# Kernel optimization log

Measured on AMD Instinct MI355X. Metric: run time of the kernel, lower is better.

Reference implementation:

```python
import jax, jax.numpy as jnp
import numpy as np

# pseudo_image_dims = [512, 512] -> canvas_x = dims[0], canvas_y = dims[1]
CANVAS_X = 512
CANVAS_Y = 512
SHIFT_SIZE = 2          # gen_index_shift(2, ...) -> 5x5 neighborhood
VR_THRESH = 0.1
B = 2
N_LI = 1_000_000
N_RA = 500_000


def setup_inputs() -> dict:
    key = jax.random.key(0)
    k1, k2, k3, k4 = jax.random.split(key, 4)
    li_input = jax.random.normal(k1, (B, N_LI, 4), dtype=jnp.float32)
    ra_input = jax.random.normal(k2, (B, N_RA, 5), dtype=jnp.float32)
    # voxel_coords (y, x) per valid point; batch column is implicitly 0
    li_coords = jax.random.randint(k3, (B, N_LI, 2), 0, CANVAS_Y).astype(jnp.int32)
    ra_coords = jax.random.randint(k4, (B, N_RA, 2), 0, CANVAS_Y).astype(jnp.int32)
    # all points valid; identity point_idxes (deterministic scatter)
    li_point_idxes = jnp.broadcast_to(jnp.arange(N_LI, dtype=jnp.int32), (B, N_LI))
    ra_point_idxes = jnp.broadcast_to(jnp.arange(N_RA, dtype=jnp.int32), (B, N_RA))
    return {
        "li_input": li_input,
        "li_coords": li_coords,
        "li_point_idxes": li_point_idxes,
        "ra_input": ra_input,
        "ra_coords": ra_coords,
        "ra_point_idxes": ra_point_idxes,
    }


def _per_batch(li_pts, li_coor, li_valid, ra_pts, ra_coor, ra_valid):
    X, Y = CANVAS_X, CANVAS_Y
    # flat BEV index per valid point: y * canvas_x + x, scattered to full point set
    li_flat = (li_coor[:, 0] * X + li_coor[:, 1]).astype(jnp.int32)
    li_ind = jnp.zeros(li_pts.shape[0], jnp.int32).at[li_valid].set(li_flat)
    ra_flat = (ra_coor[:, 0] * X + ra_coor[:, 1]).astype(jnp.int32)
    ra_ind = jnp.zeros(ra_pts.shape[0], jnp.int32).at[ra_valid].set(ra_flat)

    vr = jnp.abs(ra_pts[:, 4])
    ra_dy = vr > VR_THRESH

    # DynamicScatter(average_points=False): per-voxel MAX of |vr|; a voxel is
    # dynamic if its max |vr| > 0.1. Empty voxels -> -inf identity -> not dynamic.
    vox_max = jax.ops.segment_max(vr[ra_valid], ra_flat, num_segments=Y * X)
    dyn = (vox_max > VR_THRESH).reshape(Y, X)

    # expand each dynamic voxel to its 5x5 neighborhood with the original's
    # wrap logic: y is modded by (dims[0]+1), x by (dims[1]+1); shifted cells
    # landing on the extra row/col (== dim) are dropped.
    ys = jnp.arange(Y, dtype=jnp.int32)[:, None]   # [Y,1]
    xs = jnp.arange(X, dtype=jnp.int32)[None, :]   # [1,X]
    neigh = jnp.zeros(Y * X, dtype=jnp.int32)
    for i in range(-SHIFT_SIZE, SHIFT_SIZE + 1):
        for j in range(-SHIFT_SIZE, SHIFT_SIZE + 1):
            sy = (ys + i) % (X + 1)   # grid_size[0] = pseudo_image_dims[0] + 1
            sx = (xs + j) % (Y + 1)   # grid_size[1] = pseudo_image_dims[1] + 1
            valid = dyn & (sy < Y) & (sx < X)      # [Y,X]
            flat = sy * X + sx                      # [Y,X]
            flat = jnp.where(valid, flat, 0)
            neigh = neigh.at[flat.reshape(-1)].max(valid.reshape(-1).astype(jnp.int32))
    neigh_mask = neigh > 0          # [Y*X] bool

    li_dy = neigh_mask[li_ind]      # points with matching flat index become dynamic
    return li_dy, li_ind, ra_dy, ra_ind


def reference(li_input, li_coords, li_point_idxes, ra_input, ra_coords, ra_point_idxes):
    return jax.vmap(_per_batch)(li_input, li_coords, li_point_idxes,
                                ra_input, ra_coords, ra_point_idxes)
```

## Files before the change

kernel.cpp:

```cpp
#include <hip/hip_runtime.h>
#include <hip/hip_bf16.h>

#define CANVAS 512
#define PLANE (CANVAS * CANVAS)
#define GRIDW 513
#define BATCH 2
#define N_LI 1000000
#define N_RA 500000

__global__ void zero_dyn(uint32_t* __restrict__ p, int nwords) {
    int i = blockIdx.x * blockDim.x + threadIdx.x;
    if (i < nwords) p[i] = 0u;
}

__global__ void ra_kernel(const float* __restrict__ ra_input,
                          const int*   __restrict__ ra_coords,
                          int* __restrict__ ra_dy_out,
                          int* __restrict__ ra_ind_out,
                          unsigned char* __restrict__ dyn) {
    int idx = blockIdx.x * blockDim.x + threadIdx.x;
    if (idx >= BATCH * N_RA) return;
    float vr = fabsf(ra_input[(size_t)idx * 5 + 4]);
    int2 c = ((const int2*)ra_coords)[idx];
    int flat = c.x * CANVAS + c.y;
    int dy = (vr > 0.1f) ? 1 : 0;
    ra_dy_out[idx]  = dy;
    ra_ind_out[idx] = flat;
    if (dy) {
        int b = idx / N_RA;
        dyn[(size_t)b * PLANE + flat] = 1;
    }
}

__global__ void dilate_kernel(const unsigned char* __restrict__ dyn,
                              unsigned char* __restrict__ neigh) {
    int idx = blockIdx.x * blockDim.x + threadIdx.x;
    if (idx >= BATCH * PLANE) return;
    int b    = idx / PLANE;
    int cell = idx - b * PLANE;
    int ty = cell >> 9;
    int tx = cell & (CANVAS - 1);
    const unsigned char* d = dyn + (size_t)b * PLANE;

    int sys[5]; int nsy = 0;
    int sxs[5]; int nsx = 0;
#pragma unroll
    for (int off = -2; off <= 2; ++off) {
        int sy = ty - off;
        if (sy < 0) sy += GRIDW;
        if (sy >= GRIDW) sy -= GRIDW;
        if (sy < CANVAS) { sys[nsy++] = sy; }
        int sx = tx - off;
        if (sx < 0) sx += GRIDW;
        if (sx >= GRIDW) sx -= GRIDW;
        if (sx < CANVAS) { sxs[nsx++] = sx; }
    }
    int acc = 0;
    for (int a = 0; a < nsy; ++a) {
        int base = sys[a] * CANVAS;
        for (int c2 = 0; c2 < nsx; ++c2) acc |= d[base + sxs[c2]];
    }
    neigh[idx] = (unsigned char)(acc ? 1 : 0);
}

__global__ void li_kernel(const int* __restrict__ li_coords,
                          const unsigned char* __restrict__ neigh,
                          int* __restrict__ li_dy_out,
                          int* __restrict__ li_ind_out) {
    int idx = blockIdx.x * blockDim.x + threadIdx.x;
    if (idx >= BATCH * N_LI) return;
    int2 c = ((const int2*)li_coords)[idx];
    int flat = c.x * CANVAS + c.y;
    int b = idx / N_LI;
    li_ind_out[idx] = flat;
    li_dy_out[idx]  = neigh[(size_t)b * PLANE + flat] ? 1 : 0;
}

extern "C" void kernel_launch(void* const* d_in, const int* in_sizes, int n_in,
                              void* d_out, int out_size, void* d_ws, size_t ws_size,
                              hipStream_t stream) {
    const int*   li_coords = (const int*)d_in[1];
    const float* ra_input  = (const float*)d_in[3];
    const int*   ra_coords = (const int*)d_in[4];

    int* out        = (int*)d_out;
    int* li_dy_out  = out;
    int* li_ind_out = out + (size_t)BATCH * N_LI;
    int* ra_dy_out  = out + (size_t)2 * BATCH * N_LI;
    int* ra_ind_out = out + (size_t)2 * BATCH * N_LI + (size_t)BATCH * N_RA;

    unsigned char* dyn   = (unsigned char*)d_ws;
    unsigned char* neigh = dyn + (size_t)BATCH * PLANE;

    const int nwords = BATCH * PLANE / 4;
    zero_dyn<<<(nwords + 255) / 256, 256, 0, stream>>>((uint32_t*)dyn, nwords);
    ra_kernel<<<(BATCH * N_RA + 255) / 256, 256, 0, stream>>>(
        ra_input, ra_coords, ra_dy_out, ra_ind_out, dyn);
    dilate_kernel<<<(BATCH * PLANE + 255) / 256, 256, 0, stream>>>(dyn, neigh);
    li_kernel<<<(BATCH * N_LI + 255) / 256, 256, 0, stream>>>(
        li_coords, neigh, li_dy_out, li_ind_out);
}
```

Baseline: 141.8 us.

## Bit-pack neighbor mask, process two points per thread with vector nontemporal IO

The dilated neighbor mask is packed into 32-bit words with a wavefront ballot, so the lidar lookup gathers from a 64KB-per-batch bitmap instead of a byte plane. The radar and lidar kernels each handle two points per thread, using 16-byte coordinate loads and 8-byte nontemporal stores. The dilate loop is branchless and fully unrolled. The aim is to cut memory traffic and cache pressure on the random gathers, in exchange for extra bit arithmetic and an assumption that the wavefront is 64 lanes wide.

```diff
diff --git a/kernel.cpp b/kernel.cpp
--- a/kernel.cpp
+++ b/kernel.cpp
@@ -1,79 +1,102 @@
 #include <hip/hip_runtime.h>
-#include <hip/hip_bf16.h>
 
 #define CANVAS 512
 #define PLANE (CANVAS * CANVAS)
+#define WORDS (PLANE / 32)
 #define GRIDW 513
 #define BATCH 2
 #define N_LI 1000000
 #define N_RA 500000
+
+typedef int int2v __attribute__((ext_vector_type(2)));
+typedef int int4v __attribute__((ext_vector_type(4)));
 
 __global__ void zero_dyn(uint32_t* __restrict__ p, int nwords) {
     int i = blockIdx.x * blockDim.x + threadIdx.x;
     if (i < nwords) p[i] = 0u;
 }
 
-__global__ void ra_kernel(const float* __restrict__ ra_input,
-                          const int*   __restrict__ ra_coords,
-                          int* __restrict__ ra_dy_out,
-                          int* __restrict__ ra_ind_out,
-                          unsigned char* __restrict__ dyn) {
-    int idx = blockIdx.x * blockDim.x + threadIdx.x;
-    if (idx >= BATCH * N_RA) return;
-    float vr = fabsf(ra_input[(size_t)idx * 5 + 4]);
-    int2 c = ((const int2*)ra_coords)[idx];
-    int flat = c.x * CANVAS + c.y;
-    int dy = (vr > 0.1f) ? 1 : 0;
-    ra_dy_out[idx]  = dy;
-    ra_ind_out[idx] = flat;
-    if (dy) {
-        int b = idx / N_RA;
-        dyn[(size_t)b * PLANE + flat] = 1;
-    }
+__global__ __launch_bounds__(256) void ra_kernel(
+        const float* __restrict__ ra_input,
+        const int*   __restrict__ ra_coords,
+        int* __restrict__ ra_dy_out,
+        int* __restrict__ ra_ind_out,
+        unsigned char* __restrict__ dyn) {
+    int i = blockIdx.x * blockDim.x + threadIdx.x;
+    if (i >= BATCH * N_RA / 2) return;
+    int4v c = __builtin_nontemporal_load((const int4v*)ra_coords + i);
+    float vr0 = fabsf(__builtin_nontemporal_load(ra_input + (size_t)i * 10 + 4));
+    float vr1 = fabsf(__builtin_nontemporal_load(ra_input + (size_t)i * 10 + 9));
+    int flat0 = c.x * CANVAS + c.y;
+    int flat1 = c.z * CANVAS + c.w;
+    int dy0 = vr0 > 0.1f ? 1 : 0;
+    int dy1 = vr1 > 0.1f ? 1 : 0;
+
+    int2v dyv;  dyv.x = dy0;   dyv.y = dy1;
+    int2v indv; indv.x = flat0; indv.y = flat1;
+    __builtin_nontemporal_store(dyv,  (int2v*)ra_dy_out + i);
+    __builtin_nontemporal_store(indv, (int2v*)ra_ind_out + i);
+
+    int b = i / (N_RA / 2);
+    unsigned char* db = dyn + (size_t)b * PLANE;
+    if (dy0) db[flat0] = 1;
+    if (dy1) db[flat1] = 1;
 }
 
-__global__ void dilate_kernel(const unsigned char* __restrict__ dyn,
-                              unsigned char* __restrict__ neigh) {
-    int idx = blockIdx.x * blockDim.x + threadIdx.x;
-    if (idx >= BATCH * PLANE) return;
-    int b    = idx / PLANE;
-    int cell = idx - b * PLANE;
+__global__ __launch_bounds__(256) void dilate_kernel(
+        const unsigned char* __restrict__ dyn,
+        uint32_t* __restrict__ neighw) {
+    int idx  = blockIdx.x * blockDim.x + threadIdx.x;
+    int b    = idx >> 18;
+    int cell = idx & (PLANE - 1);
     int ty = cell >> 9;
     int tx = cell & (CANVAS - 1);
     const unsigned char* d = dyn + (size_t)b * PLANE;
 
-    int sys[5]; int nsy = 0;
-    int sxs[5]; int nsx = 0;
+    int acc = 0;
 #pragma unroll
     for (int off = -2; off <= 2; ++off) {
         int sy = ty - off;
-        if (sy < 0) sy += GRIDW;
-        if (sy >= GRIDW) sy -= GRIDW;
-        if (sy < CANVAS) { sys[nsy++] = sy; }
-        int sx = tx - off;
-        if (sx < 0) sx += GRIDW;
-        if (sx >= GRIDW) sx -= GRIDW;
-        if (sx < CANVAS) { sxs[nsx++] = sx; }
+        sy += (sy < 0)      ? GRIDW : 0;
+        sy -= (sy >= GRIDW) ? GRIDW : 0;
+        bool vy = (sy < CANVAS);
+        int rowbase = (vy ? sy : 0) * CANVAS;
+#pragma unroll
+        for (int off2 = -2; off2 <= 2; ++off2) {
+            int sx = tx - off2;
+            sx += (sx < 0)      ? GRIDW : 0;
+            sx -= (sx >= GRIDW) ? GRIDW : 0;
+            bool vx = (sx < CANVAS);
+            int v = d[rowbase + (vx ? sx : 0)];
+            acc |= (vy && vx) ? v : 0;
+        }
     }
-    int acc = 0;
-    for (int a = 0; a < nsy; ++a) {
-        int base = sys[a] * CANVAS;
-        for (int c2 = 0; c2 < nsx; ++c2) acc |= d[base + sxs[c2]];
-    }
-    neigh[idx] = (unsigned char)(acc ? 1 : 0);
+    unsigned long long m = __ballot(acc != 0);
+    int lane = threadIdx.x & 63;
+    if (lane == 0)       neighw[idx >> 5] = (uint32_t)m;
+    else if (lane == 32) neighw[idx >> 5] = (uint32_t)(m >> 32);
 }
 
-__global__ void li_kernel(const int* __restrict__ li_coords,
-                          const unsigned char* __restrict__ neigh,
-                          int* __restrict__ li_dy_out,
-                          int* __restrict__ li_ind_out) {
-    int idx = blockIdx.x * blockDim.x + threadIdx.x;
-    if (idx >= BATCH * N_LI) return;
-    int2 c = ((const int2*)li_coords)[idx];
-    int flat = c.x * CANVAS + c.y;
-    int b = idx / N_LI;
-    li_ind_out[idx] = flat;
-    li_dy_out[idx]  = neigh[(size_t)b * PLANE + flat] ? 1 : 0;
+__global__ __launch_bounds__(256) void li_kernel(
+        const int* __restrict__ li_coords,
+        const uint32_t* __restrict__ neighw,
+        int* __restrict__ li_dy_out,
+        int* __restrict__ li_ind_out) {
+    int i = blockIdx.x * blockDim.x + threadIdx.x;
+    if (i >= BATCH * N_LI / 2) return;
+    int4v c = __builtin_nontemporal_load((const int4v*)li_coords + i);
+    int flat0 = c.x * CANVAS + c.y;
+    int flat1 = c.z * CANVAS + c.w;
+    int b = i / (N_LI / 2);
+    const uint32_t* nb = neighw + (size_t)b * WORDS;
+    uint32_t w0 = nb[flat0 >> 5];
+    uint32_t w1 = nb[flat1 >> 5];
+    int2v dyv;
+    dyv.x = (int)((w0 >> (flat0 & 31)) & 1u);
+    dyv.y = (int)((w1 >> (flat1 & 31)) & 1u);
+    int2v indv; indv.x = flat0; indv.y = flat1;
+    __builtin_nontemporal_store(indv, (int2v*)li_ind_out + i);
+    __builtin_nontemporal_store(dyv,  (int2v*)li_dy_out + i);
 }
 
 extern "C" void kernel_launch(void* const* d_in, const int* in_sizes, int n_in,
@@ -89,14 +112,19 @@
     int* ra_dy_out  = out + (size_t)2 * BATCH * N_LI;
     int* ra_ind_out = out + (size_t)2 * BATCH * N_LI + (size_t)BATCH * N_RA;
 
-    unsigned char* dyn   = (unsigned char*)d_ws;
-    unsigned char* neigh = dyn + (size_t)BATCH * PLANE;
+    unsigned char* dyn    = (unsigned char*)d_ws;
+    uint32_t*      neighw = (uint32_t*)(dyn + (size_t)BATCH * PLANE);
 
     const int nwords = BATCH * PLANE / 4;
     zero_dyn<<<(nwords + 255) / 256, 256, 0, stream>>>((uint32_t*)dyn, nwords);
-    ra_kernel<<<(BATCH * N_RA + 255) / 256, 256, 0, stream>>>(
+
+    const int ra_pairs = BATCH * N_RA / 2;
+    ra_kernel<<<(ra_pairs + 255) / 256, 256, 0, stream>>>(
         ra_input, ra_coords, ra_dy_out, ra_ind_out, dyn);
-    dilate_kernel<<<(BATCH * PLANE + 255) / 256, 256, 0, stream>>>(dyn, neigh);
-    li_kernel<<<(BATCH * N_LI + 255) / 256, 256, 0, stream>>>(
-        li_coords, neigh, li_dy_out, li_ind_out);
+
+    dilate_kernel<<<BATCH * PLANE / 256, 256, 0, stream>>>(dyn, neighw);
+
+    const int li_pairs = BATCH * N_LI / 2;
+    li_kernel<<<(li_pairs + 255) / 256, 256, 0, stream>>>(
+        li_coords, neighw, li_dy_out, li_ind_out);
 }
```

New measurement: 132.7 us. -6.5%, faster.
